# Optimization experiments

Hardware: AMD Instinct MI355X
Metric: run time of the kernel (lower is better)

The kernel has to match this reference:

```python
import jax, jax.numpy as jnp
import numpy as np

D_MODEL = 256
NHEAD = 8
D_FF = 2 * D_MODEL
N_LAYERS = 4
LAYER_NAMES = ("self", "cross", "self", "cross")
EPS_ATTN = 1e-6
EPS_LN = 1e-5


def pos_encoding(x):
    # LoFTR-style 2D sinusoidal positional encoding, x: [N, C, H, W]
    n, c, h, w = x.shape
    d4 = c // 4
    # exp(arange(0, c//2, 2) * (-log(1e4) / (c//2)))
    div = jnp.exp(jnp.arange(d4, dtype=jnp.float32) * 2.0 * (-np.log(10000.0) / (c // 2)))
    xs = jnp.arange(w, dtype=jnp.float32)[None, None, :]   # [1,1,W]
    ys = jnp.arange(h, dtype=jnp.float32)[None, :, None]   # [1,H,1]
    dv = div[:, None, None]                                 # [d4,1,1]
    sx = jnp.broadcast_to(jnp.sin(xs * dv), (d4, h, w))
    cx = jnp.broadcast_to(jnp.cos(xs * dv), (d4, h, w))
    sy = jnp.broadcast_to(jnp.sin(ys * dv), (d4, h, w))
    cy = jnp.broadcast_to(jnp.cos(ys * dv), (d4, h, w))
    pe = jnp.stack([sx, cx, sy, cy], axis=1).reshape(c, h, w)  # channel order pe[0::4]=sin_x,...
    return x + pe[None]


def linear_attention(q, k, v):
    # q: [N,L,H,d], k/v: [N,S,H,d]
    Q = jax.nn.elu(q) + 1.0
    K = jax.nn.elu(k) + 1.0
    KV = jnp.einsum('nshd,nshm->nhmd', K, v)                 # [N,H,d,d]
    Z = 1.0 / (jnp.einsum('nlhd,nhd->nlh', Q, K.sum(axis=1)) + EPS_ATTN)
    return jnp.einsum('nlhd,nhmd,nlh->nlhm', Q, KV, Z)       # [N,L,H,d]


def layer_norm(x, g, b):
    m = jnp.mean(x, axis=-1, keepdims=True)
    v = jnp.mean(jnp.square(x - m), axis=-1, keepdims=True)
    return (x - m) / jnp.sqrt(v + EPS_LN) * g + b


def encoder_layer(x, src, p):
    N, L, _ = x.shape
    q = (x @ p['Wq'] + p['bq']).reshape(N, L, NHEAD, -1)
    S = src.shape[1]
    k = (src @ p['Wk'] + p['bk']).reshape(N, S, NHEAD, -1)
    v = (src @ p['Wv'] + p['bv']).reshape(N, S, NHEAD, -1)
    attn = linear_attention(q, k, v).reshape(N, L, -1) @ p['Wo'] + p['bo']
    x = layer_norm(x + attn, p['g1'], p['be1'])
    y = jax.nn.relu(x @ p['W1'] + p['b1']) @ p['W2'] + p['b2']
    return layer_norm(x + y, p['g2'], p['be2'])


def _params_at(i, Wq, bq, Wk, bk, Wv, bv, Wo, bo, W1, b1, W2, b2, g1, be1, g2, be2):
    return dict(Wq=Wq[i], bq=bq[i], Wk=Wk[i], bk=bk[i], Wv=Wv[i], bv=bv[i],
                Wo=Wo[i], bo=bo[i], W1=W1[i], b1=b1[i], W2=W2[i], b2=b2[i],
                g1=g1[i], be1=be1[i], g2=g2[i], be2=be2[i])


def setup_inputs() -> dict:
    key = jax.random.key(0)
    ks = jax.random.split(key, 16)
    N, C, H, W = 4, D_MODEL, 64, 64
    d, dff, Ln = D_MODEL, D_FF, N_LAYERS
    s = 1.0 / np.sqrt(d)
    sf = 1.0 / np.sqrt(dff)
    return {
        'ref_feature': jax.random.normal(ks[0], (N, C, H, W), jnp.float32),
        'src_feature': jax.random.normal(ks[1], (N, C, H, W), jnp.float32),
        'Wq': jax.random.normal(ks[2], (Ln, d, d), jnp.float32) * s,
        'bq': jnp.zeros((Ln, d), jnp.float32),
        'Wk': jax.random.normal(ks[3], (Ln, d, d), jnp.float32) * s,
        'bk': jnp.zeros((Ln, d), jnp.float32),
        'Wv': jax.random.normal(ks[4], (Ln, d, d), jnp.float32) * s,
        'bv': jnp.zeros((Ln, d), jnp.float32),
        'Wo': jax.random.normal(ks[5], (Ln, d, d), jnp.float32) * s,
        'bo': jnp.zeros((Ln, d), jnp.float32),
        'W1': jax.random.normal(ks[6], (Ln, d, dff), jnp.float32) * s,
        'b1': jnp.zeros((Ln, dff), jnp.float32),
        'W2': jax.random.normal(ks[7], (Ln, dff, d), jnp.float32) * sf,
        'b2': jnp.zeros((Ln, d), jnp.float32),
        'g1': jnp.ones((Ln, d), jnp.float32),
        'be1': jnp.zeros((Ln, d), jnp.float32),
        'g2': jnp.ones((Ln, d), jnp.float32),
        'be2': jnp.zeros((Ln, d), jnp.float32),
    }


def reference(ref_feature, src_feature, Wq, bq, Wk, bk, Wv, bv, Wo, bo,
              W1, b1, W2, b2, g1, be1, g2, be2):
    # FMT.forward(feat='cross')
    N, C, H, W = ref_feature.shape
    f0 = pos_encoding(ref_feature).transpose(0, 2, 3, 1).reshape(N, H * W, C)
    f1 = pos_encoding(src_feature).transpose(0, 2, 3, 1).reshape(N, H * W, C)
    p1 = jnp.concatenate([f0, f1], axis=0)   # [2N, L, C]
    p2 = jnp.concatenate([f1, f0], axis=0)
    for i, name in enumerate(LAYER_NAMES):
        p = _params_at(i, Wq, bq, Wk, bk, Wv, bv, Wo, bo, W1, b1, W2, b2, g1, be1, g2, be2)
        src = p1 if name == 'self' else p2
        p1 = encoder_layer(p1, src, p)
    out = p1.reshape(2 * N, H, W, C).transpose(0, 3, 1, 2)  # [2N, C, H, W]
    return out
```

## Files before the change

### kernel.cpp

```cpp
#include <hip/hip_runtime.h>
#include <hip/hip_bf16.h>

typedef __bf16 bf16;
typedef __attribute__((ext_vector_type(8))) __bf16 bf16x8;
typedef __attribute__((ext_vector_type(4))) __bf16 bf16x4;
typedef __attribute__((ext_vector_type(4))) float f32x4;

__device__ __forceinline__ bf16 f2bf(float f) { return (bf16)f; }

__device__ __forceinline__ void async_cp16(const void* g, void* l) {
    __builtin_amdgcn_global_load_lds(
        (const __attribute__((address_space(1))) unsigned int*)g,
        (__attribute__((address_space(3))) unsigned int*)l, 16, 0, 0);
}

__device__ __forceinline__ float pe_val(int c, int t) {
    int h = t >> 6, w = t & 63;
    int i = c >> 2, j = c & 3;
    float div = expf(-0.14391156831212787f * (float)i);
    float arg = ((j < 2) ? (float)w : (float)h) * div;
    return (j & 1) ? cosf(arg) : sinf(arg);
}

__global__ __launch_bounds__(1024) void encode_kernel(const float* __restrict__ ref,
                                                      const float* __restrict__ src,
                                                      bf16* __restrict__ Xb,
                                                      bf16* __restrict__ P2b) {
    __shared__ float tile[32][33];
    int n = blockIdx.z >> 1, sel = blockIdx.z & 1;
    const float* f = sel ? src : ref;
    int t = blockIdx.x * 32 + threadIdx.x;
    int c = blockIdx.y * 32 + threadIdx.y;
    float v = f[((size_t)n * 256 + c) * 4096 + t] + pe_val(c, t);
    tile[threadIdx.y][threadIdx.x] = v;
    __syncthreads();
    int tt = blockIdx.x * 32 + threadIdx.y;
    int cc = blockIdx.y * 32 + threadIdx.x;
    float o = tile[threadIdx.x][threadIdx.y];
    int bx = sel ? 4 + n : n;
    int bp = sel ? n : 4 + n;
    Xb [((size_t)bx * 4096 + tt) * 256 + cc] = f2bf(o);
    P2b[((size_t)bp * 4096 + tt) * 256 + cc] = f2bf(o);
}

__global__ __launch_bounds__(1024) void wt_conv(const float* __restrict__ Wq, const float* __restrict__ Wk,
                                                const float* __restrict__ Wv, const float* __restrict__ Wo,
                                                const float* __restrict__ W1, const float* __restrict__ W2,
                                                bf16* __restrict__ Wt) {
    __shared__ float t[32][33];
    int z = blockIdx.z, L = z / 6, m = z - L * 6;
    const float* src; int K, N, doff;
    if      (m == 0) { src = Wq + L * 65536;  K = 256; N = 256; doff = 0; }
    else if (m == 1) { src = Wk + L * 65536;  K = 256; N = 256; doff = 65536; }
    else if (m == 2) { src = Wv + L * 65536;  K = 256; N = 256; doff = 131072; }
    else if (m == 3) { src = Wo + L * 65536;  K = 256; N = 256; doff = 196608; }
    else if (m == 4) { src = W1 + L * 131072; K = 256; N = 512; doff = 262144; }
    else             { src = W2 + L * 131072; K = 512; N = 256; doff = 393216; }
    int n0 = blockIdx.x * 32, k0 = blockIdx.y * 32;
    if (n0 >= N || k0 >= K) return;
    t[threadIdx.y][threadIdx.x] = src[(size_t)(k0 + threadIdx.y) * N + n0 + threadIdx.x];
    __syncthreads();
    bf16* dst = Wt + (size_t)L * 524288 + doff;
    dst[(size_t)(n0 + threadIdx.y) * K + k0 + threadIdx.x] = f2bf(t[threadIdx.x][threadIdx.y]);
}

__global__ __launch_bounds__(256) void gemm_qkv(const bf16* __restrict__ Aq,
                                                const bf16* __restrict__ Akv,
                                                const bf16* __restrict__ Wt,
                                                const float* __restrict__ bq,
                                                const float* __restrict__ bk,
                                                const float* __restrict__ bv,
                                                bf16* __restrict__ Q,
                                                bf16* __restrict__ Ko,
                                                bf16* __restrict__ V) {
    __shared__ bf16 Als[2][128 * 64];
    __shared__ bf16 Bls[2][128 * 64];
    int tid = threadIdx.x;
    int wave = tid >> 6, lane = tid & 63;
    int id = blockIdx.x;
    int swz = (id & 7) * 192 + (id >> 3);
    int bm = (swz / 6) * 128, bn = (swz % 6) * 128;
    int wm = (wave >> 1) * 64, wn = (wave & 1) * 64;
    int l15 = lane & 15, g = lane >> 4;
    const int K = 256;

    int seg = bn >> 8, cloc = bn & 255;
    const bf16* A = seg == 0 ? Aq : Akv;
    const float* bias = seg == 0 ? bq : (seg == 1 ? bk : bv);
    bf16* Out = seg == 0 ? Q : (seg == 1 ? Ko : V);
    bool do_elu = seg < 2;

    f32x4 acc[4][4] = {};

#define QKV_STAGE(buf, k0)                                                      \
    {                                                                           \
        _Pragma("unroll")                                                       \
        for (int r = 0; r < 4; ++r) {                                           \
            int Lc = r * 256 + tid;                                             \
            int row = Lc >> 3, cs = Lc & 7;                                     \
            int gc = cs ^ (row & 7);                                            \
            async_cp16(A  + (size_t)(bm + row) * K + (k0) + gc * 8, &Als[buf][Lc * 8]); \
            async_cp16(Wt + (size_t)(bn + row) * K + (k0) + gc * 8, &Bls[buf][Lc * 8]); \
        }                                                                       \
    }

    QKV_STAGE(0, 0);
    __syncthreads();
    int cur = 0;
    for (int t = 0; t < 4; ++t) {
        if (t < 3) QKV_STAGE(cur ^ 1, (t + 1) * 64);
#pragma unroll
        for (int ks = 0; ks < 2; ++ks) {
            bf16x8 af[4], bfr[4];
#pragma unroll
            for (int i = 0; i < 4; ++i) {
                int row = wm + i * 16 + l15;
                int c = ks * 4 + g;
                af[i] = *(bf16x8*)&Als[cur][row * 64 + ((c ^ (row & 7)) * 8)];
            }
#pragma unroll
            for (int j = 0; j < 4; ++j) {
                int row = wn + j * 16 + l15;
                int c = ks * 4 + g;
                bfr[j] = *(bf16x8*)&Bls[cur][row * 64 + ((c ^ (row & 7)) * 8)];
            }
#pragma unroll
            for (int i = 0; i < 4; ++i)
#pragma unroll
                for (int j = 0; j < 4; ++j)
                    acc[i][j] = __builtin_amdgcn_mfma_f32_16x16x32_bf16(af[i], bfr[j], acc[i][j], 0, 0, 0);
        }
        __syncthreads();
        cur ^= 1;
    }
#undef QKV_STAGE

    int r4 = (lane >> 4) * 4;
#pragma unroll
    for (int i = 0; i < 4; ++i) {
#pragma unroll
        for (int j = 0; j < 4; ++j) {
            int cj = cloc + wn + j * 16 + l15;
            float bvv = bias[cj];
#pragma unroll
            for (int r = 0; r < 4; ++r) {
                int row = bm + wm + i * 16 + r4 + r;
                float v = acc[i][j][r] + bvv;
                if (do_elu) v = v > 0.f ? v + 1.f : expf(v);
                Out[(size_t)row * 256 + cj] = f2bf(v);
            }
        }
    }
}

template <int RELU>
__global__ __launch_bounds__(256) void gemm_mfma(const bf16* __restrict__ A,
                                                 const bf16* __restrict__ Wt,
                                                 const float* __restrict__ bias,
                                                 bf16* __restrict__ C,
                                                 int N, int K, int nbn) {
    __shared__ bf16 Als[2][128 * 64];
    __shared__ bf16 Bls[2][128 * 64];
    int tid = threadIdx.x;
    int wave = tid >> 6, lane = tid & 63;
    int id = blockIdx.x;
    int nwg = gridDim.x;
    int cpx = nwg >> 3;
    int swz = (id & 7) * cpx + (id >> 3);
    int bm = (swz / nbn) * 128, bn = (swz % nbn) * 128;
    int wm = (wave >> 1) * 64, wn = (wave & 1) * 64;
    int l15 = lane & 15, g = lane >> 4;

    f32x4 acc[4][4] = {};

#define MF_STAGE(buf, k0)                                                       \
    {                                                                           \
        _Pragma("unroll")                                                       \
        for (int r = 0; r < 4; ++r) {                                           \
            int Lc = r * 256 + tid;                                             \
            int row = Lc >> 3, cs = Lc & 7;                                     \
            int gc = cs ^ (row & 7);                                            \
            async_cp16(A  + (size_t)(bm + row) * K + (k0) + gc * 8, &Als[buf][Lc * 8]); \
            async_cp16(Wt + (size_t)(bn + row) * K + (k0) + gc * 8, &Bls[buf][Lc * 8]); \
        }                                                                       \
    }

    int nt = K >> 6;
    MF_STAGE(0, 0);
    __syncthreads();
    int cur = 0;
    for (int t = 0; t < nt; ++t) {
        if (t < nt - 1) MF_STAGE(cur ^ 1, (t + 1) * 64);
#pragma unroll
        for (int ks = 0; ks < 2; ++ks) {
            bf16x8 af[4], bfr[4];
#pragma unroll
            for (int i = 0; i < 4; ++i) {
                int row = wm + i * 16 + l15;
                int c = ks * 4 + g;
                af[i] = *(bf16x8*)&Als[cur][row * 64 + ((c ^ (row & 7)) * 8)];
            }
#pragma unroll
            for (int j = 0; j < 4; ++j) {
                int row = wn + j * 16 + l15;
                int c = ks * 4 + g;
                bfr[j] = *(bf16x8*)&Bls[cur][row * 64 + ((c ^ (row & 7)) * 8)];
            }
#pragma unroll
            for (int i = 0; i < 4; ++i)
#pragma unroll
                for (int j = 0; j < 4; ++j)
                    acc[i][j] = __builtin_amdgcn_mfma_f32_16x16x32_bf16(af[i], bfr[j], acc[i][j], 0, 0, 0);
        }
        __syncthreads();
        cur ^= 1;
    }
#undef MF_STAGE

    int r4 = (lane >> 4) * 4;
#pragma unroll
    for (int i = 0; i < 4; ++i) {
#pragma unroll
        for (int j = 0; j < 4; ++j) {
            int col = bn + wn + j * 16 + l15;
            float bvv = bias[col];
#pragma unroll
            for (int r = 0; r < 4; ++r) {
                int row = bm + wm + i * 16 + r4 + r;
                float v = acc[i][j][r] + bvv;
                if (RELU) v = fmaxf(v, 0.f);
                C[(size_t)row * N + col] = f2bf(v);
            }
        }
    }
}

__global__ __launch_bounds__(512) void gemm_ln(const bf16* __restrict__ A,
                                               const bf16* __restrict__ Wt,
                                               const float* __restrict__ bias,
                                               bf16* __restrict__ Xb,
                                               const float* __restrict__ g,
                                               const float* __restrict__ b,
                                               int K) {
    __shared__ __align__(16) char smem[128 * 260 * 2];
    bf16* Als = (bf16*)smem;
    bf16* Bls = (bf16*)(smem + 16384);
    bf16* Cls = (bf16*)smem;

    int tid = threadIdx.x;
    int wave = tid >> 6, lane = tid & 63;
    int bm = blockIdx.x * 128;
    int wm = (wave >> 2) * 64, wn = (wave & 3) * 64;
    int l15 = lane & 15, gg = lane >> 4;

    f32x4 acc[4][4] = {};

    for (int k0 = 0; k0 < K; k0 += 64) {
#pragma unroll
        for (int r = 0; r < 2; ++r) {
            int Lc = r * 512 + tid;
            int row = Lc >> 3, cs = Lc & 7;
            int gc = cs ^ (row & 7);
            async_cp16(A + (size_t)(bm + row) * K + k0 + gc * 8, &Als[Lc * 8]);
        }
#pragma unroll
        for (int r = 0; r < 4; ++r) {
            int Lc = r * 512 + tid;
            int row = Lc >> 3, cs = Lc & 7;
            int gc = cs ^ (row & 7);
            async_cp16(Wt + (size_t)row * K + k0 + gc * 8, &Bls[Lc * 8]);
        }
        __syncthreads();
#pragma unroll
        for (int ks = 0; ks < 2; ++ks) {
            bf16x8 af[4], bfr[4];
#pragma unroll
            for (int i = 0; i < 4; ++i) {
                int row = wm + i * 16 + l15;
                int c = ks * 4 + gg;
                af[i] = *(bf16x8*)&Als[row * 64 + ((c ^ (row & 7)) * 8)];
            }
#pragma unroll
            for (int j = 0; j < 4; ++j) {
                int row = wn + j * 16 + l15;
                int c = ks * 4 + gg;
                bfr[j] = *(bf16x8*)&Bls[row * 64 + ((c ^ (row & 7)) * 8)];
            }
#pragma unroll
            for (int i = 0; i < 4; ++i)
#pragma unroll
                for (int j = 0; j < 4; ++j)
                    acc[i][j] = __builtin_amdgcn_mfma_f32_16x16x32_bf16(af[i], bfr[j], acc[i][j], 0, 0, 0);
        }
        __syncthreads();
    }

    int r4 = (lane >> 4) * 4;
#pragma unroll
    for (int j = 0; j < 4; ++j) {
        int col = wn + j * 16 + l15;
        float bvv = bias[col];
#pragma unroll
        for (int i = 0; i < 4; ++i)
#pragma unroll
            for (int r = 0; r < 4; ++r)
                Cls[(wm + i * 16 + r4 + r) * 260 + col] = f2bf(acc[i][j][r] + bvv);
    }
    __syncthreads();

    int c4 = lane * 4;
    float4 gw = *(const float4*)&g[c4];
    float4 bw = *(const float4*)&b[c4];
#pragma unroll 2
    for (int rw = 0; rw < 16; ++rw) {
        int row = wave * 16 + rw;
        size_t gidx = (size_t)(bm + row) * 256 + c4;
        bf16x4 xb = *(const bf16x4*)(Xb + gidx);
        bf16x4 cb = *(const bf16x4*)&Cls[row * 260 + c4];
        float4 v;
        v.x = (float)xb[0] + (float)cb[0];
        v.y = (float)xb[1] + (float)cb[1];
        v.z = (float)xb[2] + (float)cb[2];
        v.w = (float)xb[3] + (float)cb[3];
        float s  = v.x + v.y + v.z + v.w;
        float sq = v.x * v.x + v.y * v.y + v.z * v.z + v.w * v.w;
#pragma unroll
        for (int off = 32; off > 0; off >>= 1) {
            s  += __shfl_xor(s,  off);
            sq += __shfl_xor(sq, off);
        }
        float mean = s * (1.f / 256.f);
        float var  = sq * (1.f / 256.f) - mean * mean;
        float rstd = rsqrtf(var + 1e-5f);
        bf16x4 ob;
        ob[0] = f2bf((v.x - mean) * rstd * gw.x + bw.x);
        ob[1] = f2bf((v.y - mean) * rstd * gw.y + bw.y);
        ob[2] = f2bf((v.z - mean) * rstd * gw.z + bw.z);
        ob[3] = f2bf((v.w - mean) * rstd * gw.w + bw.w);
        *(bf16x4*)(Xb + gidx) = ob;
    }
}

__global__ __launch_bounds__(512) void gemm_attn_ln(const bf16* __restrict__ A,
                                                    const float* __restrict__ Ksum,
                                                    const bf16* __restrict__ Weff,
                                                    const float* __restrict__ bias,
                                                    bf16* __restrict__ Xb,
                                                    const float* __restrict__ g,
                                                    const float* __restrict__ b) {
    __shared__ __align__(16) char smem[128 * 260 * 2];
    bf16*  Als = (bf16*)smem;
    bf16*  Bls = (bf16*)(smem + 16384);
    float* Zs  = (float*)(smem + 49152);
    bf16*  Cls = (bf16*)smem;

    int tid = threadIdx.x;
    int wave = tid >> 6, lane = tid & 63;
    int bm = blockIdx.x * 128;
    int n = bm >> 12;
    const bf16* Wt = Weff + (size_t)n * 65536;

    {
        int row = tid >> 2, part = tid & 3;
        const bf16* qp = A + (size_t)(bm + row) * 256 + part * 64;
        const float* kp = Ksum + n * 256 + part * 64;
#pragma unroll
        for (int hh = 0; hh < 2; ++hh) {
            float p[8];
#pragma unroll
            for (int i = 0; i < 8; ++i) {
                bf16x4 q = *(const bf16x4*)(qp + hh * 32 + i * 4);
                float4 k = *(const float4*)(kp + hh * 32 + i * 4);
                p[i] = (float)q[0] * k.x + (float)q[1] * k.y
                     + (float)q[2] * k.z + (float)q[3] * k.w;
            }
            float z = ((p[0] + p[1]) + (p[2] + p[3])) + ((p[4] + p[5]) + (p[6] + p[7]));
            Zs[row * 8 + part * 2 + hh] = 1.f / (z + 1e-6f);
        }
    }
    __syncthreads();

    int wm = (wave >> 2) * 64, wn = (wave & 3) * 64;
    int l15 = lane & 15, gg = lane >> 4;

    f32x4 acc[4][4] = {};

    for (int k0 = 0; k0 < 256; k0 += 64) {
#pragma unroll
        for (int r = 0; r < 4; ++r) {
            int Lc = r * 512 + tid;
            int row = Lc >> 3, cs = Lc & 7;
            int gc = cs ^ (row & 7);
            async_cp16(Wt + (size_t)row * 256 + k0 + gc * 8, &Bls[Lc * 8]);
        }
#pragma unroll
        for (int r = 0; r < 2; ++r) {
            int Lc = r * 512 + tid;
            int row = Lc >> 3, cs = Lc & 7;
            int gc = cs ^ (row & 7);
            int gcol = k0 + gc * 8;
            bf16x8 q8 = *(const bf16x8*)(A + (size_t)(bm + row) * 256 + gcol);
            float z = Zs[row * 8 + (gcol >> 5)];
            bf16x8 a8;
#pragma unroll
            for (int u = 0; u < 8; ++u) a8[u] = f2bf((float)q8[u] * z);
            *(bf16x8*)&Als[Lc * 8] = a8;
        }
        __syncthreads();
#pragma unroll
        for (int ks = 0; ks < 2; ++ks) {
            bf16x8 af[4], bfr[4];
#pragma unroll
            for (int i = 0; i < 4; ++i) {
                int row = wm + i * 16 + l15;
                int c = ks * 4 + gg;
                af[i] = *(bf16x8*)&Als[row * 64 + ((c ^ (row & 7)) * 8)];
            }
#pragma unroll
            for (int j = 0; j < 4; ++j) {
                int row = wn + j * 16 + l15;
                int c = ks * 4 + gg;
                bfr[j] = *(bf16x8*)&Bls[row * 64 + ((c ^ (row & 7)) * 8)];
            }
#pragma unroll
            for (int i = 0; i < 4; ++i)
#pragma unroll
                for (int j = 0; j < 4; ++j)
                    acc[i][j] = __builtin_amdgcn_mfma_f32_16x16x32_bf16(af[i], bfr[j], acc[i][j], 0, 0, 0);
        }
        __syncthreads();
    }

    int r4 = (lane >> 4) * 4;
#pragma unroll
    for (int j = 0; j < 4; ++j) {
        int col = wn + j * 16 + l15;
        float bvv = bias[col];
#pragma unroll
        for (int i = 0; i < 4; ++i)
#pragma unroll
            for (int r = 0; r < 4; ++r)
                Cls[(wm + i * 16 + r4 + r) * 260 + col] = f2bf(acc[i][j][r] + bvv);
    }
    __syncthreads();

    int c4 = lane * 4;
    float4 gw = *(const float4*)&g[c4];
    float4 bw = *(const float4*)&b[c4];
#pragma unroll 2
    for (int rw = 0; rw < 16; ++rw) {
        int row = wave * 16 + rw;
        size_t gidx = (size_t)(bm + row) * 256 + c4;
        bf16x4 xb = *(const bf16x4*)(Xb + gidx);
        bf16x4 cb = *(const bf16x4*)&Cls[row * 260 + c4];
        float4 v;
        v.x = (float)xb[0] + (float)cb[0];
        v.y = (float)xb[1] + (float)cb[1];
        v.z = (float)xb[2] + (float)cb[2];
        v.w = (float)xb[3] + (float)cb[3];
        float s  = v.x + v.y + v.z + v.w;
        float sq = v.x * v.x + v.y * v.y + v.z * v.z + v.w * v.w;
#pragma unroll
        for (int off = 32; off > 0; off >>= 1) {
            s  += __shfl_xor(s,  off);
            sq += __shfl_xor(sq, off);
        }
        float mean = s * (1.f / 256.f);
        float var  = sq * (1.f / 256.f) - mean * mean;
        float rstd = rsqrtf(var + 1e-5f);
        bf16x4 ob;
        ob[0] = f2bf((v.x - mean) * rstd * gw.x + bw.x);
        ob[1] = f2bf((v.y - mean) * rstd * gw.y + bw.y);
        ob[2] = f2bf((v.z - mean) * rstd * gw.z + bw.z);
        ob[3] = f2bf((v.w - mean) * rstd * gw.w + bw.w);
        *(bf16x4*)(Xb + gidx) = ob;
    }
}

__global__ __launch_bounds__(256) void kv_prep_part(const bf16* __restrict__ Kb,
                                                    const bf16* __restrict__ Vb,
                                                    float* __restrict__ Pkv,
                                                    float* __restrict__ Pks) {
    __shared__ float Ks[128][32];
    __shared__ float Vs[128][32];
    int sp = blockIdx.x;
    int nh = blockIdx.y;
    int n = nh >> 3, h = nh & 7;
    int tid = threadIdx.x;
    int wave = tid >> 6, lane = tid & 63;
    int mg = lane >> 3;
    int dg = lane & 7;
    size_t base = ((size_t)n * 4096 + sp * 128) * 256 + h * 32;

#pragma unroll
    for (int p = 0; p < 2; ++p) {
        int r = p * 64 + (tid >> 2);
        int c = (tid & 3) * 8;
        bf16x8 k8 = *(const bf16x8*)(Kb + base + (size_t)r * 256 + c);
        bf16x8 v8 = *(const bf16x8*)(Vb + base + (size_t)r * 256 + c);
#pragma unroll
        for (int u = 0; u < 8; ++u) { Ks[r][c + u] = (float)k8[u]; Vs[r][c + u] = (float)v8[u]; }
    }
    __syncthreads();

    float acc[4][4] = {};
    float ks4[4] = {};
    int s0 = wave * 32;
    for (int s = s0; s < s0 + 32; ++s) {
        float4 kq = *(float4*)&Ks[s][dg * 4];
        float4 vq = *(float4*)&Vs[s][mg * 4];
        ks4[0] += kq.x; ks4[1] += kq.y; ks4[2] += kq.z; ks4[3] += kq.w;
        acc[0][0] += vq.x * kq.x; acc[0][1] += vq.x * kq.y; acc[0][2] += vq.x * kq.z; acc[0][3] += vq.x * kq.w;
        acc[1][0] += vq.y * kq.x; acc[1][1] += vq.y * kq.y; acc[1][2] += vq.y * kq.z; acc[1][3] += vq.y * kq.w;
        acc[2][0] += vq.z * kq.x; acc[2][1] += vq.z * kq.y; acc[2][2] += vq.z * kq.z; acc[2][3] += vq.z * kq.w;
        acc[3][0] += vq.w * kq.x; acc[3][1] += vq.w * kq.y; acc[3][2] += vq.w * kq.z; acc[3][3] += vq.w * kq.w;
    }
    __syncthreads();

    float* R  = &Ks[0][0];
    float* RS = &Vs[0][0];
#pragma unroll
    for (int mi = 0; mi < 4; ++mi)
#pragma unroll
        for (int dj = 0; dj < 4; ++dj)
            R[wave * 1024 + (mg * 4 + mi) * 32 + dg * 4 + dj] = acc[mi][dj];
    if (mg == 0)
#pragma unroll
        for (int dj = 0; dj < 4; ++dj) RS[wave * 32 + dg * 4 + dj] = ks4[dj];
    __syncthreads();

    int e = tid * 4;
    float4 o0 = *(float4*)&R[e];
    float4 o1 = *(float4*)&R[1024 + e];
    float4 o2 = *(float4*)&R[2048 + e];
    float4 o3 = *(float4*)&R[3072 + e];
    float4 o = make_float4(o0.x + o1.x + o2.x + o3.x, o0.y + o1.y + o2.y + o3.y,
                           o0.z + o1.z + o2.z + o3.z, o0.w + o1.w + o2.w + o3.w);
    *(float4*)&Pkv[((size_t)nh * 32 + sp) * 1024 + e] = o;
    if (tid < 32)
        Pks[((size_t)nh * 32 + sp) * 32 + tid] = RS[tid] + RS[32 + tid] + RS[64 + tid] + RS[96 + tid];
}

__global__ __launch_bounds__(64) void kv_reduce(const float* __restrict__ Pkv,
                                                const float* __restrict__ Pks,
                                                float* __restrict__ KV,
                                                float* __restrict__ Ksum) {
    int nh = blockIdx.x;
    int q = blockIdx.y;
    int e = (q * 64 + threadIdx.x) * 4;
    float4 s = make_float4(0.f, 0.f, 0.f, 0.f);
    for (int sp = 0; sp < 32; ++sp) {
        float4 p = *(const float4*)&Pkv[((size_t)nh * 32 + sp) * 1024 + e];
        s.x += p.x; s.y += p.y; s.z += p.z; s.w += p.w;
    }
    *(float4*)&KV[(size_t)nh * 1024 + e] = s;
    if (q == 0 && threadIdx.x < 32) {
        float ss = 0.f;
        for (int sp = 0; sp < 32; ++sp) ss += Pks[((size_t)nh * 32 + sp) * 32 + threadIdx.x];
        Ksum[nh * 32 + threadIdx.x] = ss;
    }
}

__global__ __launch_bounds__(256) void weff_kernel(const float* __restrict__ KV,
                                                   const bf16* __restrict__ WtO,
                                                   bf16* __restrict__ Weff) {
    __shared__ float KVs[8][1024];
    int n = blockIdx.y, c0 = blockIdx.x * 64;
    int tid = threadIdx.x;
    const float* src = KV + (size_t)n * 8192;
    for (int i = tid; i < 2048; i += 256)
        *(float4*)&((float*)KVs)[i * 4] = *(const float4*)&src[i * 4];
    __syncthreads();

    int c = c0 + (tid & 63);
    int hb = tid >> 6;
    const bf16* wrow = WtO + (size_t)c * 256 + hb * 64;
    bf16* dst = Weff + (size_t)n * 65536 + (size_t)c * 256 + hb * 64;

#pragma unroll
    for (int hh = 0; hh < 2; ++hh) {
        int h = hb * 2 + hh;
        float wo[32];
#pragma unroll
        for (int u = 0; u < 4; ++u) {
            bf16x8 w8 = *(const bf16x8*)(wrow + hh * 32 + u * 8);
#pragma unroll
            for (int v = 0; v < 8; ++v) wo[u * 8 + v] = (float)w8[v];
        }
        float s[32] = {};
        for (int m = 0; m < 32; ++m) {
            float wm = wo[m];
#pragma unroll
            for (int d4 = 0; d4 < 8; ++d4) {
                float4 kv4 = *(float4*)&KVs[h][m * 32 + d4 * 4];
                s[d4 * 4 + 0] += wm * kv4.x;
                s[d4 * 4 + 1] += wm * kv4.y;
                s[d4 * 4 + 2] += wm * kv4.z;
                s[d4 * 4 + 3] += wm * kv4.w;
            }
        }
#pragma unroll
        for (int u = 0; u < 4; ++u) {
            bf16x8 o8;
#pragma unroll
            for (int v = 0; v < 8; ++v) o8[v] = f2bf(s[u * 8 + v]);
            *(bf16x8*)(dst + hh * 32 + u * 8) = o8;
        }
    }
}

__global__ __launch_bounds__(1024) void store_kernel(const bf16* __restrict__ Xb,
                                                     float* __restrict__ out) {
    __shared__ float tile[32][33];
    int b = blockIdx.z;
    int t0 = blockIdx.x * 32, c0 = blockIdx.y * 32;
    tile[threadIdx.y][threadIdx.x] =
        (float)Xb[((size_t)b * 4096 + t0 + threadIdx.y) * 256 + c0 + threadIdx.x];
    __syncthreads();
    out[((size_t)b * 256 + c0 + threadIdx.y) * 4096 + t0 + threadIdx.x] =
        tile[threadIdx.x][threadIdx.y];
}

extern "C" void kernel_launch(void* const* d_in, const int* in_sizes, int n_in,
                              void* d_out, int out_size, void* d_ws, size_t ws_size,
                              hipStream_t stream) {
    const float* ref  = (const float*)d_in[0];
    const float* srcf = (const float*)d_in[1];
    const float* Wq = (const float*)d_in[2];
    const float* bq = (const float*)d_in[3];
    const float* Wk = (const float*)d_in[4];
    const float* bk = (const float*)d_in[5];
    const float* Wv = (const float*)d_in[6];
    const float* bv = (const float*)d_in[7];
    const float* Wo = (const float*)d_in[8];
    const float* bo = (const float*)d_in[9];
    const float* W1 = (const float*)d_in[10];
    const float* b1 = (const float*)d_in[11];
    const float* W2 = (const float*)d_in[12];
    const float* b2 = (const float*)d_in[13];
    const float* g1 = (const float*)d_in[14];
    const float* be1 = (const float*)d_in[15];
    const float* g2 = (const float*)d_in[16];
    const float* be2 = (const float*)d_in[17];

    const size_t SZ = (size_t)8 * 4096 * 256;
    float* ws  = (float*)d_ws;
    float* KVb = ws;
    float* Ksb = KVb + 65536;
    float* Pkv = Ksb + 2048;
    float* Pks = Pkv + 2097152;
    bf16*  Wt  = (bf16*)(Pks + 65536);
    bf16*  Xb  = Wt + 2097152;
    bf16*  P2b = Xb + SZ;
    bf16*  Qb  = P2b + SZ;
    bf16*  Weffb = (bf16*)Pkv;
    bf16*  Kb  = (bf16*)d_out;
    bf16*  Vb  = Kb + SZ;
    bf16*  Hb  = Kb;

    wt_conv<<<dim3(16, 16, 24), dim3(32, 32), 0, stream>>>(Wq, Wk, Wv, Wo, W1, W2, Wt);
    encode_kernel<<<dim3(128, 8, 8), dim3(32, 32), 0, stream>>>(ref, srcf, Xb, P2b);

    for (int L = 0; L < 4; ++L) {
        const bf16* WtL = Wt + (size_t)L * 524288;
        const bf16* Akv = (L & 1) ? P2b : Xb;
        gemm_qkv<<<1536, 256, 0, stream>>>(Xb, Akv, WtL,
                                           bq + L * 256, bk + L * 256, bv + L * 256,
                                           Qb, Kb, Vb);
        kv_prep_part<<<dim3(32, 64), 256, 0, stream>>>(Kb, Vb, Pkv, Pks);
        kv_reduce<<<dim3(64, 4), 64, 0, stream>>>(Pkv, Pks, KVb, Ksb);
        weff_kernel<<<dim3(4, 8), 256, 0, stream>>>(KVb, WtL + 196608, Weffb);
        gemm_attn_ln<<<256, 512, 0, stream>>>(Qb, Ksb, Weffb, bo + L * 256, Xb,
                                              g1 + L * 256, be1 + L * 256);
        gemm_mfma<1><<<1024, 256, 0, stream>>>(Xb, WtL + 262144, b1 + L * 512, Hb, 512, 256, 4);
        gemm_ln<<<256, 512, 0, stream>>>(Hb, WtL + 393216, b2 + L * 256, Xb,
                                         g2 + L * 256, be2 + L * 256, 512);
    }

    store_kernel<<<dim3(128, 8, 8), dim3(32, 32), 0, stream>>>(Xb, (float*)d_out);
}
```

Baseline: 665.3 us.

## Double-buffer LDS tiles in the GEMM+LayerNorm kernels to overlap loads with MFMA

Result: faster. 647.6 us (-2.7%).

```diff
diff --git a/kernel.cpp b/kernel.cpp
--- a/kernel.cpp
+++ b/kernel.cpp
@@ -242,9 +242,7 @@
                                                const float* __restrict__ g,
                                                const float* __restrict__ b,
                                                int K) {
-    __shared__ __align__(16) char smem[128 * 260 * 2];
-    bf16* Als = (bf16*)smem;
-    bf16* Bls = (bf16*)(smem + 16384);
+    __shared__ __align__(16) char smem[98304];
     bf16* Cls = (bf16*)smem;
 
     int tid = threadIdx.x;
@@ -255,22 +253,34 @@
 
     f32x4 acc[4][4] = {};
 
-    for (int k0 = 0; k0 < K; k0 += 64) {
-#pragma unroll
-        for (int r = 0; r < 2; ++r) {
-            int Lc = r * 512 + tid;
-            int row = Lc >> 3, cs = Lc & 7;
-            int gc = cs ^ (row & 7);
-            async_cp16(A + (size_t)(bm + row) * K + k0 + gc * 8, &Als[Lc * 8]);
-        }
-#pragma unroll
-        for (int r = 0; r < 4; ++r) {
-            int Lc = r * 512 + tid;
-            int row = Lc >> 3, cs = Lc & 7;
-            int gc = cs ^ (row & 7);
-            async_cp16(Wt + (size_t)row * K + k0 + gc * 8, &Bls[Lc * 8]);
-        }
-        __syncthreads();
+#define LN_ALS(buf) ((bf16*)(smem + (buf) * 16384))
+#define LN_BLS(buf) ((bf16*)(smem + 32768 + (buf) * 32768))
+#define LN_STAGE(buf, k0)                                                       \
+    {                                                                           \
+        _Pragma("unroll")                                                       \
+        for (int r = 0; r < 2; ++r) {                                           \
+            int Lc = r * 512 + tid;                                             \
+            int row = Lc >> 3, cs = Lc & 7;                                     \
+            int gc = cs ^ (row & 7);                                            \
+            async_cp16(A + (size_t)(bm + row) * K + (k0) + gc * 8, &LN_ALS(buf)[Lc * 8]); \
+        }                                                                       \
+        _Pragma("unroll")                                                       \
+        for (int r = 0; r < 4; ++r) {                                           \
+            int Lc = r * 512 + tid;                                             \
+            int row = Lc >> 3, cs = Lc & 7;                                     \
+            int gc = cs ^ (row & 7);                                            \
+            async_cp16(Wt + (size_t)row * K + (k0) + gc * 8, &LN_BLS(buf)[Lc * 8]); \
+        }                                                                       \
+    }
+
+    int nt = K >> 6;
+    LN_STAGE(0, 0);
+    __syncthreads();
+    int cur = 0;
+    for (int t = 0; t < nt; ++t) {
+        if (t < nt - 1) LN_STAGE(cur ^ 1, (t + 1) * 64);
+        const bf16* Als = LN_ALS(cur);
+        const bf16* Bls = LN_BLS(cur);
 #pragma unroll
         for (int ks = 0; ks < 2; ++ks) {
             bf16x8 af[4], bfr[4];
@@ -293,7 +303,11 @@
                     acc[i][j] = __builtin_amdgcn_mfma_f32_16x16x32_bf16(af[i], bfr[j], acc[i][j], 0, 0, 0);
         }
         __syncthreads();
-    }
+        cur ^= 1;
+    }
+#undef LN_STAGE
+#undef LN_ALS
+#undef LN_BLS
 
     int r4 = (lane >> 4) * 4;
 #pragma unroll
@@ -348,11 +362,9 @@
                                                     bf16* __restrict__ Xb,
                                                     const float* __restrict__ g,
                                                     const float* __restrict__ b) {
-    __shared__ __align__(16) char smem[128 * 260 * 2];
-    bf16*  Als = (bf16*)smem;
-    bf16*  Bls = (bf16*)(smem + 16384);
-    float* Zs  = (float*)(smem + 49152);
+    __shared__ __align__(16) char smem[102400];
     bf16*  Cls = (bf16*)smem;
+    float* Zs  = (float*)(smem + 98304);
 
     int tid = threadIdx.x;
     int wave = tid >> 6, lane = tid & 63;
@@ -385,28 +397,39 @@
 
     f32x4 acc[4][4] = {};
 
-    for (int k0 = 0; k0 < 256; k0 += 64) {
-#pragma unroll
-        for (int r = 0; r < 4; ++r) {
-            int Lc = r * 512 + tid;
-            int row = Lc >> 3, cs = Lc & 7;
-            int gc = cs ^ (row & 7);
-            async_cp16(Wt + (size_t)row * 256 + k0 + gc * 8, &Bls[Lc * 8]);
-        }
-#pragma unroll
-        for (int r = 0; r < 2; ++r) {
-            int Lc = r * 512 + tid;
-            int row = Lc >> 3, cs = Lc & 7;
-            int gc = cs ^ (row & 7);
-            int gcol = k0 + gc * 8;
-            bf16x8 q8 = *(const bf16x8*)(A + (size_t)(bm + row) * 256 + gcol);
-            float z = Zs[row * 8 + (gcol >> 5)];
-            bf16x8 a8;
-#pragma unroll
-            for (int u = 0; u < 8; ++u) a8[u] = f2bf((float)q8[u] * z);
-            *(bf16x8*)&Als[Lc * 8] = a8;
-        }
-        __syncthreads();
+#define AT_ALS(buf) ((bf16*)(smem + (buf) * 16384))
+#define AT_BLS(buf) ((bf16*)(smem + 32768 + (buf) * 32768))
+#define AT_STAGE(buf, k0)                                                       \
+    {                                                                           \
+        _Pragma("unroll")                                                       \
+        for (int r = 0; r < 4; ++r) {                                           \
+            int Lc = r * 512 + tid;                                             \
+            int row = Lc >> 3, cs = Lc & 7;                                     \
+            int gc = cs ^ (row & 7);                                            \
+            async_cp16(Wt + (size_t)row * 256 + (k0) + gc * 8, &AT_BLS(buf)[Lc * 8]); \
+        }                                                                       \
+        _Pragma("unroll")                                                       \
+        for (int r = 0; r < 2; ++r) {                                           \
+            int Lc = r * 512 + tid;                                             \
+            int row = Lc >> 3, cs = Lc & 7;                                     \
+            int gc = cs ^ (row & 7);                                            \
+            int gcol = (k0) + gc * 8;                                           \
+            bf16x8 q8 = *(const bf16x8*)(A + (size_t)(bm + row) * 256 + gcol);  \
+            float z = Zs[row * 8 + (gcol >> 5)];                                \
+            bf16x8 a8;                                                          \
+            _Pragma("unroll")                                                   \
+            for (int u = 0; u < 8; ++u) a8[u] = f2bf((float)q8[u] * z);         \
+            *(bf16x8*)&AT_ALS(buf)[Lc * 8] = a8;                                \
+        }                                                                       \
+    }
+
+    AT_STAGE(0, 0);
+    __syncthreads();
+    int cur = 0;
+    for (int t = 0; t < 4; ++t) {
+        if (t < 3) AT_STAGE(cur ^ 1, (t + 1) * 64);
+        const bf16* Als = AT_ALS(cur);
+        const bf16* Bls = AT_BLS(cur);
 #pragma unroll
         for (int ks = 0; ks < 2; ++ks) {
             bf16x8 af[4], bfr[4];
@@ -429,7 +452,11 @@
                     acc[i][j] = __builtin_amdgcn_mfma_f32_16x16x32_bf16(af[i], bfr[j], acc[i][j], 0, 0, 0);
         }
         __syncthreads();
-    }
+        cur ^= 1;
+    }
+#undef AT_STAGE
+#undef AT_ALS
+#undef AT_BLS
 
     int r4 = (lane >> 4) * 4;
 #pragma unroll
```
